# Optimization experiments

Hardware: AMD Instinct MI355X
Metric: run time of the kernel (lower is better)

The kernel has to match this reference:

```python
import jax, jax.numpy as jnp
import numpy as np

B, T, C = 4, 4096, 1024
DIM_K, DIM_V = 64, 64


def setup_inputs() -> dict:
    key = jax.random.key(0)
    k1, k2, k3, k4, k5, k6 = jax.random.split(key, 6)
    q_embs = jax.random.normal(k1, (B, T, C), dtype=jnp.float32)
    k_embs = jax.random.normal(k2, (B, T, C), dtype=jnp.float32)
    v_embs = jax.random.normal(k3, (B, T, C), dtype=jnp.float32)
    # nn.Linear(C, dim) weights have shape (dim, C); y = x @ W.T
    s = 1.0 / np.sqrt(C)
    w_q = jax.random.uniform(k4, (DIM_K, C), jnp.float32, -s, s)
    w_k = jax.random.uniform(k5, (DIM_K, C), jnp.float32, -s, s)
    w_v = jax.random.uniform(k6, (DIM_V, C), jnp.float32, -s, s)
    return {"q_embs": q_embs, "k_embs": k_embs, "v_embs": v_embs,
            "w_q": w_q, "w_k": w_k, "w_v": w_v}


def reference(q_embs, k_embs, v_embs, w_q, w_k, w_v):
    Bv, Tv, Cv = v_embs.shape
    q = jnp.einsum('btc,kc->btk', q_embs, w_q)  # [B,T,dim_k]
    k = jnp.einsum('btc,kc->btk', k_embs, w_k)  # [B,T,dim_k]
    v = jnp.einsum('btc,vc->btv', v_embs, w_v)  # [B,T,dim_v]
    # NOTE: original scales by C**-0.5 (embedding dim), not dim_k**-0.5
    scores = jnp.einsum('bqk,bsk->bqs', q, k) * (Cv ** -0.5)  # [B,T,T]
    causal = jnp.tril(jnp.ones((Tv, Tv), dtype=bool))
    scores = jnp.where(causal, scores, -jnp.inf)
    wei = jax.nn.softmax(scores, axis=-1)
    return jnp.einsum('bqs,bsv->bqv', wei, v)  # [B,T,dim_v]
```

## Files before the change

kernel.cpp:

```cpp
#include <hip/hip_runtime.h>

#define TSEQ 4096
#define CDIM 1024
#define DHEAD 64

typedef __bf16 bf16x8 __attribute__((ext_vector_type(8)));
typedef float f32x4 __attribute__((ext_vector_type(4)));

#define KCHUNK 128
#define NCHUNK (CDIM / KCHUNK)
#define LSTRIDE 136

__global__ __launch_bounds__(256) void proj_kernel(
    const float* __restrict__ qe, const float* __restrict__ ke,
    const float* __restrict__ ve, const float* __restrict__ wq,
    const float* __restrict__ wk, const float* __restrict__ wv,
    __bf16* __restrict__ Qo, __bf16* __restrict__ Ko, __bf16* __restrict__ Vto)
{
  __shared__ __bf16 Al[64][LSTRIDE];
  __shared__ __bf16 Wl[64][LSTRIDE];

  const int pid = blockIdx.y;
  const float* __restrict__ emb = (pid == 0) ? qe : ((pid == 1) ? ke : ve);
  const float* __restrict__ W   = (pid == 0) ? wq : ((pid == 1) ? wk : wv);
  const int wave = threadIdx.x >> 6;
  const int lane = threadIdx.x & 63;
  const int g = lane >> 4, c = lane & 15;
  const int bm0 = blockIdx.x * 64;

  const int lr = lane >> 5;
  const int lc = (lane & 31) * 4;

  const float* __restrict__ ebase = emb + (size_t)(bm0 + wave * 16 + lr) * CDIM + lc;
  const float* __restrict__ wbase = W + (size_t)(wave * 16 + lr) * CDIM + lc;

  f32x4 acc[4];
#pragma unroll
  for (int n = 0; n < 4; ++n) acc[n] = (f32x4){0.f, 0.f, 0.f, 0.f};

  f32x4 ra[8], rw[8];
#pragma unroll
  for (int j = 0; j < 8; ++j) {
    ra[j] = *(const f32x4*)(ebase + (size_t)(2 * j) * CDIM);
    rw[j] = *(const f32x4*)(wbase + (size_t)(2 * j) * CDIM);
  }

  for (int ch = 0; ch < NCHUNK; ++ch) {
    __syncthreads();
#pragma unroll
    for (int j = 0; j < 8; ++j) {
      const int row = wave * 16 + 2 * j + lr;
      short4 pa, pw;
      pa.x = __builtin_bit_cast(short, (__bf16)ra[j][0]);
      pa.y = __builtin_bit_cast(short, (__bf16)ra[j][1]);
      pa.z = __builtin_bit_cast(short, (__bf16)ra[j][2]);
      pa.w = __builtin_bit_cast(short, (__bf16)ra[j][3]);
      pw.x = __builtin_bit_cast(short, (__bf16)rw[j][0]);
      pw.y = __builtin_bit_cast(short, (__bf16)rw[j][1]);
      pw.z = __builtin_bit_cast(short, (__bf16)rw[j][2]);
      pw.w = __builtin_bit_cast(short, (__bf16)rw[j][3]);
      *(short4*)&Al[row][lc] = pa;
      *(short4*)&Wl[row][lc] = pw;
    }
    if (ch + 1 < NCHUNK) {
      const float* __restrict__ e2 = ebase + (size_t)(ch + 1) * KCHUNK;
      const float* __restrict__ w2 = wbase + (size_t)(ch + 1) * KCHUNK;
#pragma unroll
      for (int j = 0; j < 8; ++j) {
        ra[j] = *(const f32x4*)(e2 + (size_t)(2 * j) * CDIM);
        rw[j] = *(const f32x4*)(w2 + (size_t)(2 * j) * CDIM);
      }
    }
    __syncthreads();
#pragma unroll
    for (int ks = 0; ks < KCHUNK / 32; ++ks) {
      bf16x8 af = *(const bf16x8*)&Al[wave * 16 + c][ks * 32 + g * 8];
#pragma unroll
      for (int n = 0; n < 4; ++n) {
        bf16x8 wf = *(const bf16x8*)&Wl[n * 16 + c][ks * 32 + g * 8];
        acc[n] = __builtin_amdgcn_mfma_f32_16x16x32_bf16(af, wf, acc[n], 0, 0, 0);
      }
    }
  }

  const int m0 = bm0 + wave * 16;
  if (pid < 2) {
    __bf16* __restrict__ dst = (pid == 0) ? Qo : Ko;
#pragma unroll
    for (int n = 0; n < 4; ++n)
#pragma unroll
      for (int r = 0; r < 4; ++r)
        dst[(size_t)(m0 + g * 4 + r) * DHEAD + n * 16 + c] = (__bf16)acc[n][r];
  } else {
    const int t0 = m0 + g * 4;
    const int bb = t0 >> 12;
    const int tl = t0 & (TSEQ - 1);
#pragma unroll
    for (int n = 0; n < 4; ++n) {
      const int v = n * 16 + c;
      ushort4 pk;
      pk.x = __builtin_bit_cast(unsigned short, (__bf16)acc[n][0]);
      pk.y = __builtin_bit_cast(unsigned short, (__bf16)acc[n][1]);
      pk.z = __builtin_bit_cast(unsigned short, (__bf16)acc[n][2]);
      pk.w = __builtin_bit_cast(unsigned short, (__bf16)acc[n][3]);
      *(ushort4*)(Vto + ((size_t)bb * DHEAD + v) * TSEQ + tl) = pk;
    }
  }
}

#define NWAVE 8

__global__ __launch_bounds__(512) void attn_kernel(
    const __bf16* __restrict__ Q, const __bf16* __restrict__ K,
    const __bf16* __restrict__ Vt, float* __restrict__ out)
{
  __shared__ __bf16 Plds[NWAVE][16][72];
  __shared__ float Om[NWAVE][16][65];
  __shared__ float La[NWAVE][16];

  const int b = blockIdx.y;
  const int tile = (int)gridDim.x - 1 - (int)blockIdx.x;
  const int q0 = tile * 16;
  const int wave = threadIdx.x >> 6;
  const int lane = threadIdx.x & 63;
  const int g = lane >> 4, c = lane & 15;

  const __bf16* Qb = Q + (size_t)b * TSEQ * DHEAD;
  const __bf16* Kb = K + (size_t)b * TSEQ * DHEAD;
  const __bf16* Vb = Vt + (size_t)b * DHEAD * TSEQ;

  bf16x8 aq0 = *(const bf16x8*)(Qb + (size_t)(q0 + c) * DHEAD + g * 8);
  bf16x8 aq1 = *(const bf16x8*)(Qb + (size_t)(q0 + c) * DHEAD + 32 + g * 8);

  bf16x8 ones;
#pragma unroll
  for (int j = 0; j < 8; ++j) ones[j] = (__bf16)1.0f;

  f32x4 o[4];
#pragma unroll
  for (int n = 0; n < 4; ++n) o[n] = (f32x4){0.f, 0.f, 0.f, 0.f};
  f32x4 lacc = (f32x4){0.f, 0.f, 0.f, 0.f};

  const float kScale = 0.04508422f;
  const int nt = (q0 + 16 + 63) >> 6;

  for (int st = wave; st < nt; st += 2 * NWAVE) {
    const int s0A = st * 64;
    const int stB = st + NWAVE;
    const bool hasB = stB < nt;
    const int s0B = stB * 64;

    bf16x8 ka0[4], ka1[4], kb0[4], kb1[4];
#pragma unroll
    for (int n = 0; n < 4; ++n) {
      const __bf16* kp = Kb + (size_t)(s0A + n * 16 + c) * DHEAD + g * 8;
      ka0[n] = *(const bf16x8*)(kp);
      ka1[n] = *(const bf16x8*)(kp + 32);
    }
    if (hasB) {
#pragma unroll
      for (int n = 0; n < 4; ++n) {
        const __bf16* kp = Kb + (size_t)(s0B + n * 16 + c) * DHEAD + g * 8;
        kb0[n] = *(const bf16x8*)(kp);
        kb1[n] = *(const bf16x8*)(kp + 32);
      }
    }

    f32x4 sA[4];
#pragma unroll
    for (int n = 0; n < 4; ++n) {
      f32x4 z = (f32x4){0.f, 0.f, 0.f, 0.f};
      z = __builtin_amdgcn_mfma_f32_16x16x32_bf16(aq0, ka0[n], z, 0, 0, 0);
      sA[n] = __builtin_amdgcn_mfma_f32_16x16x32_bf16(aq1, ka1[n], z, 0, 0, 0);
    }
    bf16x8 va0[4], va1[4];
#pragma unroll
    for (int n = 0; n < 4; ++n) {
      const __bf16* vp = Vb + (size_t)(n * 16 + c) * TSEQ + s0A + g * 8;
      va0[n] = *(const bf16x8*)(vp);
      va1[n] = *(const bf16x8*)(vp + 32);
    }
#pragma unroll
    for (int n = 0; n < 4; ++n) {
      const int sidx = s0A + n * 16 + c;
#pragma unroll
      for (int r = 0; r < 4; ++r) {
        const int qidx = q0 + g * 4 + r;
        float p = (sidx <= qidx) ? __builtin_amdgcn_exp2f(sA[n][r] * kScale) : 0.f;
        Plds[wave][g * 4 + r][n * 16 + c] = (__bf16)p;
      }
    }

    f32x4 sB[4];
    bf16x8 vb0[4], vb1[4];
    if (hasB) {
#pragma unroll
      for (int n = 0; n < 4; ++n) {
        f32x4 z = (f32x4){0.f, 0.f, 0.f, 0.f};
        z = __builtin_amdgcn_mfma_f32_16x16x32_bf16(aq0, kb0[n], z, 0, 0, 0);
        sB[n] = __builtin_amdgcn_mfma_f32_16x16x32_bf16(aq1, kb1[n], z, 0, 0, 0);
      }
#pragma unroll
      for (int n = 0; n < 4; ++n) {
        const __bf16* vp = Vb + (size_t)(n * 16 + c) * TSEQ + s0B + g * 8;
        vb0[n] = *(const bf16x8*)(vp);
        vb1[n] = *(const bf16x8*)(vp + 32);
      }
    }

    bf16x8 p0A = *(const bf16x8*)(&Plds[wave][c][g * 8]);
    bf16x8 p1A = *(const bf16x8*)(&Plds[wave][c][32 + g * 8]);
    lacc = __builtin_amdgcn_mfma_f32_16x16x32_bf16(p0A, ones, lacc, 0, 0, 0);
    lacc = __builtin_amdgcn_mfma_f32_16x16x32_bf16(p1A, ones, lacc, 0, 0, 0);

    if (hasB) {
#pragma unroll
      for (int n = 0; n < 4; ++n) {
        const int sidx = s0B + n * 16 + c;
#pragma unroll
        for (int r = 0; r < 4; ++r) {
          const int qidx = q0 + g * 4 + r;
          float p = (sidx <= qidx) ? __builtin_amdgcn_exp2f(sB[n][r] * kScale) : 0.f;
          Plds[wave][g * 4 + r][n * 16 + c] = (__bf16)p;
        }
      }
    }

#pragma unroll
    for (int n = 0; n < 4; ++n) {
      o[n] = __builtin_amdgcn_mfma_f32_16x16x32_bf16(p0A, va0[n], o[n], 0, 0, 0);
      o[n] = __builtin_amdgcn_mfma_f32_16x16x32_bf16(p1A, va1[n], o[n], 0, 0, 0);
    }

    if (hasB) {
      bf16x8 p0B = *(const bf16x8*)(&Plds[wave][c][g * 8]);
      bf16x8 p1B = *(const bf16x8*)(&Plds[wave][c][32 + g * 8]);
      lacc = __builtin_amdgcn_mfma_f32_16x16x32_bf16(p0B, ones, lacc, 0, 0, 0);
      lacc = __builtin_amdgcn_mfma_f32_16x16x32_bf16(p1B, ones, lacc, 0, 0, 0);
#pragma unroll
      for (int n = 0; n < 4; ++n) {
        o[n] = __builtin_amdgcn_mfma_f32_16x16x32_bf16(p0B, vb0[n], o[n], 0, 0, 0);
        o[n] = __builtin_amdgcn_mfma_f32_16x16x32_bf16(p1B, vb1[n], o[n], 0, 0, 0);
      }
    }
  }

#pragma unroll
  for (int n = 0; n < 4; ++n)
#pragma unroll
    for (int r = 0; r < 4; ++r)
      Om[wave][g * 4 + r][n * 16 + c] = o[n][r];
  if (c == 0) {
#pragma unroll
    for (int r = 0; r < 4; ++r) La[wave][g * 4 + r] = lacc[r];
  }
  __syncthreads();

  const int tid = threadIdx.x;
  const int q = tid >> 5;
  const int c2 = (tid & 31) * 2;
  float l = 0.f;
#pragma unroll
  for (int w = 0; w < NWAVE; ++w) l += La[w][q];
  float s0 = 0.f, s1 = 0.f;
#pragma unroll
  for (int w = 0; w < NWAVE; ++w) {
    s0 += Om[w][q][c2];
    s1 += Om[w][q][c2 + 1];
  }
  const float inv = 1.0f / l;
  float2 r;
  r.x = s0 * inv;
  r.y = s1 * inv;
  *(float2*)(out + ((size_t)b * TSEQ + q0 + q) * DHEAD + c2) = r;
}

extern "C" void kernel_launch(void* const* d_in, const int* in_sizes, int n_in,
                              void* d_out, int out_size, void* d_ws, size_t ws_size,
                              hipStream_t stream) {
  const float* qe = (const float*)d_in[0];
  const float* ke = (const float*)d_in[1];
  const float* ve = (const float*)d_in[2];
  const float* wq = (const float*)d_in[3];
  const float* wk = (const float*)d_in[4];
  const float* wv = (const float*)d_in[5];

  __bf16* Qw  = (__bf16*)d_ws;
  __bf16* Kw  = Qw + (size_t)4 * TSEQ * DHEAD;
  __bf16* Vtw = Kw + (size_t)4 * TSEQ * DHEAD;

  dim3 g1(4 * TSEQ / 64, 3), b1(256);
  proj_kernel<<<g1, b1, 0, stream>>>(qe, ke, ve, wq, wk, wv, Qw, Kw, Vtw);

  dim3 g2(TSEQ / 16, 4), b2(512);
  attn_kernel<<<g2, b2, 0, stream>>>(Qw, Kw, Vtw, (float*)d_out);
}
```

Measured before the change: 281.3 us.

## Pre-convert weights to bf16 and load projection operands directly into registers

A small kernel now converts the three projection weight matrices to bf16 once per call, into workspace. The projection kernel drops shared-memory staging and block barriers. Each lane loads its fp32 embedding fragment straight into registers through a three-deep chunk pipeline and reads bf16 weight fragments directly from global memory. This removes LDS traffic and sync cost, at the price of an extra launch and redundant per-wave weight reads served from cache.

```diff
diff --git a/kernel.cpp b/kernel.cpp
--- a/kernel.cpp
+++ b/kernel.cpp
@@ -9,81 +9,91 @@
 
 #define KCHUNK 128
 #define NCHUNK (CDIM / KCHUNK)
-#define LSTRIDE 136
+
+__global__ __launch_bounds__(256) void wconv_kernel(
+    const float* __restrict__ wq, const float* __restrict__ wk,
+    const float* __restrict__ wv, __bf16* __restrict__ Wb)
+{
+  const int t = blockIdx.x * 256 + threadIdx.x;
+  const int idx = t * 8;
+  const int pid = idx >> 16;
+  const float* __restrict__ src = (pid == 0) ? wq : ((pid == 1) ? wk : wv);
+  const int off = idx & 65535;
+  f32x4 a = *(const f32x4*)(src + off);
+  f32x4 b = *(const f32x4*)(src + off + 4);
+  ushort4 lo, hi;
+  lo.x = __builtin_bit_cast(unsigned short, (__bf16)a[0]);
+  lo.y = __builtin_bit_cast(unsigned short, (__bf16)a[1]);
+  lo.z = __builtin_bit_cast(unsigned short, (__bf16)a[2]);
+  lo.w = __builtin_bit_cast(unsigned short, (__bf16)a[3]);
+  hi.x = __builtin_bit_cast(unsigned short, (__bf16)b[0]);
+  hi.y = __builtin_bit_cast(unsigned short, (__bf16)b[1]);
+  hi.z = __builtin_bit_cast(unsigned short, (__bf16)b[2]);
+  hi.w = __builtin_bit_cast(unsigned short, (__bf16)b[3]);
+  *(ushort4*)(Wb + idx) = lo;
+  *(ushort4*)(Wb + idx + 4) = hi;
+}
 
 __global__ __launch_bounds__(256) void proj_kernel(
     const float* __restrict__ qe, const float* __restrict__ ke,
-    const float* __restrict__ ve, const float* __restrict__ wq,
-    const float* __restrict__ wk, const float* __restrict__ wv,
+    const float* __restrict__ ve, const __bf16* __restrict__ Wb,
     __bf16* __restrict__ Qo, __bf16* __restrict__ Ko, __bf16* __restrict__ Vto)
 {
-  __shared__ __bf16 Al[64][LSTRIDE];
-  __shared__ __bf16 Wl[64][LSTRIDE];
-
   const int pid = blockIdx.y;
   const float* __restrict__ emb = (pid == 0) ? qe : ((pid == 1) ? ke : ve);
-  const float* __restrict__ W   = (pid == 0) ? wq : ((pid == 1) ? wk : wv);
+  const __bf16* __restrict__ W = Wb + (size_t)pid * DHEAD * CDIM;
+
   const int wave = threadIdx.x >> 6;
   const int lane = threadIdx.x & 63;
   const int g = lane >> 4, c = lane & 15;
-  const int bm0 = blockIdx.x * 64;
-
-  const int lr = lane >> 5;
-  const int lc = (lane & 31) * 4;
-
-  const float* __restrict__ ebase = emb + (size_t)(bm0 + wave * 16 + lr) * CDIM + lc;
-  const float* __restrict__ wbase = W + (size_t)(wave * 16 + lr) * CDIM + lc;
+  const int m0 = blockIdx.x * 64 + wave * 16;
+
+  const float* __restrict__ arow = emb + (size_t)(m0 + c) * CDIM + g * 8;
+  const __bf16* __restrict__ wbase = W + (size_t)c * CDIM + g * 8;
 
   f32x4 acc[4];
 #pragma unroll
   for (int n = 0; n < 4; ++n) acc[n] = (f32x4){0.f, 0.f, 0.f, 0.f};
 
-  f32x4 ra[8], rw[8];
-#pragma unroll
-  for (int j = 0; j < 8; ++j) {
-    ra[j] = *(const f32x4*)(ebase + (size_t)(2 * j) * CDIM);
-    rw[j] = *(const f32x4*)(wbase + (size_t)(2 * j) * CDIM);
-  }
-
+  auto loadA = [&](f32x4* L, f32x4* H, int ch) {
+#pragma unroll
+    for (int ks = 0; ks < 4; ++ks) {
+      const float* p = arow + ch * KCHUNK + ks * 32;
+      L[ks] = *(const f32x4*)(p);
+      H[ks] = *(const f32x4*)(p + 4);
+    }
+  };
+  auto compute = [&](const f32x4* L, const f32x4* H, int ch) {
+#pragma unroll
+    for (int ks = 0; ks < 4; ++ks) {
+      bf16x8 af;
+      af[0] = (__bf16)L[ks][0];
+      af[1] = (__bf16)L[ks][1];
+      af[2] = (__bf16)L[ks][2];
+      af[3] = (__bf16)L[ks][3];
+      af[4] = (__bf16)H[ks][0];
+      af[5] = (__bf16)H[ks][1];
+      af[6] = (__bf16)H[ks][2];
+      af[7] = (__bf16)H[ks][3];
+      const __bf16* wp = wbase + ch * KCHUNK + ks * 32;
+#pragma unroll
+      for (int n = 0; n < 4; ++n) {
+        bf16x8 wf = *(const bf16x8*)(wp + (size_t)n * 16 * CDIM);
+        acc[n] = __builtin_amdgcn_mfma_f32_16x16x32_bf16(af, wf, acc[n], 0, 0, 0);
+      }
+    }
+  };
+
+  f32x4 L[3][4], H[3][4];
+  loadA(L[0], H[0], 0);
+  loadA(L[1], H[1], 1);
+  loadA(L[2], H[2], 2);
+#pragma unroll
   for (int ch = 0; ch < NCHUNK; ++ch) {
-    __syncthreads();
-#pragma unroll
-    for (int j = 0; j < 8; ++j) {
-      const int row = wave * 16 + 2 * j + lr;
-      short4 pa, pw;
-      pa.x = __builtin_bit_cast(short, (__bf16)ra[j][0]);
-      pa.y = __builtin_bit_cast(short, (__bf16)ra[j][1]);
-      pa.z = __builtin_bit_cast(short, (__bf16)ra[j][2]);
-      pa.w = __builtin_bit_cast(short, (__bf16)ra[j][3]);
-      pw.x = __builtin_bit_cast(short, (__bf16)rw[j][0]);
-      pw.y = __builtin_bit_cast(short, (__bf16)rw[j][1]);
-      pw.z = __builtin_bit_cast(short, (__bf16)rw[j][2]);
-      pw.w = __builtin_bit_cast(short, (__bf16)rw[j][3]);
-      *(short4*)&Al[row][lc] = pa;
-      *(short4*)&Wl[row][lc] = pw;
-    }
-    if (ch + 1 < NCHUNK) {
-      const float* __restrict__ e2 = ebase + (size_t)(ch + 1) * KCHUNK;
-      const float* __restrict__ w2 = wbase + (size_t)(ch + 1) * KCHUNK;
-#pragma unroll
-      for (int j = 0; j < 8; ++j) {
-        ra[j] = *(const f32x4*)(e2 + (size_t)(2 * j) * CDIM);
-        rw[j] = *(const f32x4*)(w2 + (size_t)(2 * j) * CDIM);
-      }
-    }
-    __syncthreads();
-#pragma unroll
-    for (int ks = 0; ks < KCHUNK / 32; ++ks) {
-      bf16x8 af = *(const bf16x8*)&Al[wave * 16 + c][ks * 32 + g * 8];
-#pragma unroll
-      for (int n = 0; n < 4; ++n) {
-        bf16x8 wf = *(const bf16x8*)&Wl[n * 16 + c][ks * 32 + g * 8];
-        acc[n] = __builtin_amdgcn_mfma_f32_16x16x32_bf16(af, wf, acc[n], 0, 0, 0);
-      }
-    }
-  }
-
-  const int m0 = bm0 + wave * 16;
+    compute(L[ch % 3], H[ch % 3], ch);
+    if (ch + 3 < NCHUNK) loadA(L[ch % 3], H[ch % 3], ch + 3);
+  }
+
   if (pid < 2) {
     __bf16* __restrict__ dst = (pid == 0) ? Qo : Ko;
 #pragma unroll
@@ -288,9 +298,12 @@
   __bf16* Qw  = (__bf16*)d_ws;
   __bf16* Kw  = Qw + (size_t)4 * TSEQ * DHEAD;
   __bf16* Vtw = Kw + (size_t)4 * TSEQ * DHEAD;
+  __bf16* Wb  = Vtw + (size_t)4 * TSEQ * DHEAD;
+
+  wconv_kernel<<<dim3(96), dim3(256), 0, stream>>>(wq, wk, wv, Wb);
 
   dim3 g1(4 * TSEQ / 64, 3), b1(256);
-  proj_kernel<<<g1, b1, 0, stream>>>(qe, ke, ve, wq, wk, wv, Qw, Kw, Vtw);
+  proj_kernel<<<g1, b1, 0, stream>>>(qe, ke, ve, Wb, Qw, Kw, Vtw);
 
   dim3 g2(TSEQ / 16, 4), b2(512);
   attn_kernel<<<g2, b2, 0, stream>>>(Qw, Kw, Vtw, (float*)d_out);
```

Measured after the change: 291.6 us. 3.7% more time.
